# Optimization experiments

Measured on AMD Instinct MI355X. Metric: run time of the kernel, lower is better.

## Reference

```python
import jax, jax.numpy as jnp
import numpy as np

B, S, D, H, HD = 8, 1, 4096, 32, 128
MAX_SEQ, AL, FF = 2048, 10, 11008
START_POS = 2047
EPS = 1e-5


def setup_inputs() -> dict:
    key = jax.random.key(0)
    ks = jax.random.split(key, 12)
    # real RoPE angles for the single decode position START_POS
    inv_freq = 1.0 / (10000.0 ** (np.arange(0, HD, 2, dtype=np.float32) / HD))  # [HD/2]
    ang = (np.float32(START_POS) * inv_freq)[None, :]  # [S=1, HD/2]
    return {
        "x": jax.random.normal(ks[0], (B, S, D), jnp.float32),
        "adapter": jax.random.normal(ks[1], (1, AL, D), jnp.float32),
        "cache_k": jax.random.normal(ks[2], (B, MAX_SEQ, H, HD), jnp.float32),
        "cache_v": jax.random.normal(ks[3], (B, MAX_SEQ, H, HD), jnp.float32),
        "freqs_cos": jnp.cos(jnp.asarray(ang)),
        "freqs_sin": jnp.sin(jnp.asarray(ang)),
        "wq": jax.random.normal(ks[4], (D, D), jnp.float32) * 0.02,
        "wk": jax.random.normal(ks[5], (D, D), jnp.float32) * 0.02,
        "wv": jax.random.normal(ks[6], (D, D), jnp.float32) * 0.02,
        "wo": jax.random.normal(ks[7], (D, D), jnp.float32) * 0.02,
        "gate": jax.random.normal(ks[8], (1, H, 1, 1), jnp.float32) * 0.5,
        "attn_norm_w": jnp.ones((D,), jnp.float32),
        "ffn_norm_w": jnp.ones((D,), jnp.float32),
        "w1": jax.random.normal(ks[9], (D, FF), jnp.float32) * 0.02,
        "w2": jax.random.normal(ks[10], (FF, D), jnp.float32) * 0.02,
        "w3": jax.random.normal(ks[11], (D, FF), jnp.float32) * 0.02,
        "start_pos": START_POS,
    }


def _rmsnorm(x, w, eps=EPS):
    xf = x.astype(jnp.float32)
    return (xf * jax.lax.rsqrt(jnp.mean(xf * xf, axis=-1, keepdims=True) + eps)).astype(x.dtype) * w


def _rope(t, cos, sin):
    # t: [B,S,H,HD]; pairs are interleaved as in view_as_complex(reshape(..,-1,2))
    tr = t.reshape(*t.shape[:-1], HD // 2, 2)
    a, b = tr[..., 0], tr[..., 1]
    c = cos[None, :, None, :]
    s = sin[None, :, None, :]
    out = jnp.stack([a * c - b * s, a * s + b * c], axis=-1)
    return out.reshape(t.shape)


def _sdpa(q, k, v):
    # q:[B,H,S,HD], k/v:[B,H,K,HD]
    scores = jnp.einsum("bhqd,bhkd->bhqk", q, k) / jnp.sqrt(jnp.float32(HD))
    p = jax.nn.softmax(scores.astype(jnp.float32), axis=-1).astype(q.dtype)
    return jnp.einsum("bhqk,bhkd->bhqd", p, v)


def reference(x, adapter, cache_k, cache_v, freqs_cos, freqs_sin,
              wq, wk, wv, wo, gate, attn_norm_w, ffn_norm_w, w1, w2, w3, start_pos):
    bsz, seqlen, _ = x.shape
    # --- attention sub-block ---
    xn = _rmsnorm(x, attn_norm_w)
    xq = (xn @ wq).reshape(bsz, seqlen, H, HD)
    xk = (xn @ wk).reshape(bsz, seqlen, H, HD)
    xv = (xn @ wv).reshape(bsz, seqlen, H, HD)
    xq = _rope(xq, freqs_cos, freqs_sin)
    xk = _rope(xk, freqs_cos, freqs_sin)
    # KV-cache append
    cache_k = jax.lax.dynamic_update_slice(cache_k, xk, (0, start_pos, 0, 0))
    cache_v = jax.lax.dynamic_update_slice(cache_v, xv, (0, start_pos, 0, 0))
    keys = cache_k[:, : start_pos + seqlen].transpose(0, 2, 1, 3)   # [B,H,K,HD]
    values = cache_v[:, : start_pos + seqlen].transpose(0, 2, 1, 3)
    q = xq.transpose(0, 2, 1, 3)                                     # [B,H,S,HD]
    out = _sdpa(q, keys, values)                                     # [B,H,S,HD]
    # adapter-gated cross attention (adapter keys/values: no RoPE, shared over batch)
    ak = (adapter @ wk).reshape(AL, H, HD).transpose(1, 0, 2)        # [H,AL,HD]
    av = (adapter @ wv).reshape(AL, H, HD).transpose(1, 0, 2)        # [H,AL,HD]
    a_scores = jnp.einsum("bhqd,hkd->bhqk", q, ak) / jnp.sqrt(jnp.float32(HD))
    a_p = jax.nn.softmax(a_scores.astype(jnp.float32), axis=-1).astype(q.dtype)
    a_out = jnp.einsum("bhqk,hkd->bhqd", a_p, av)
    out = out + jnp.tanh(gate) * a_out
    attn_out = out.transpose(0, 2, 1, 3).reshape(bsz, seqlen, H * HD) @ wo
    h = x + attn_out
    # --- feed-forward sub-block (SwiGLU) ---
    hn = _rmsnorm(h, ffn_norm_w)
    ffn = (jax.nn.silu(hn @ w1) * (hn @ w3)) @ w2
    return h + ffn
```

## Files before the change

kernel.cpp:

```cpp
#include <hip/hip_runtime.h>
#include <cmath>

#define D_ 4096
#define H_ 32
#define HD_ 128
#define B_ 8
#define MAXSEQ_ 2048
#define AL_ 10
#define FF_ 11008
#define SCALE_ 0.08838834764831845f
#define EPS_ 1e-5f

__global__ __launch_bounds__(256) void norm_adapter_k(const float* __restrict__ x,
                                                      const float* __restrict__ w,
                                                      const float* __restrict__ adapter,
                                                      float* __restrict__ xa) {
  int b = blockIdx.x, tid = threadIdx.x;
  if (b < 8) {
    const float* xr = x + (size_t)b * D_;
    float ss = 0.f;
    for (int i = tid; i < D_; i += 256) { float v = xr[i]; ss += v * v; }
    __shared__ float red[256];
    red[tid] = ss; __syncthreads();
    for (int s = 128; s; s >>= 1) { if (tid < s) red[tid] += red[tid + s]; __syncthreads(); }
    float r = rsqrtf(red[0] / (float)D_ + EPS_);
    float* o = xa + (size_t)b * D_;
    for (int i = tid; i < D_; i += 256) o[i] = xr[i] * r * w[i];
  } else {
    int r = b - 8;
    const float4* src = (const float4*)(adapter + (size_t)r * D_);
    float4* dst = (float4*)(xa + (size_t)(8 + r) * D_);
    for (int i = tid; i < D_ / 4; i += 256) dst[i] = src[i];
  }
}

__global__ __launch_bounds__(256) void rmsnorm_k(const float* __restrict__ in,
                                                 const float* __restrict__ w,
                                                 float* __restrict__ out) {
  int b = blockIdx.x, tid = threadIdx.x;
  const float* x = in + (size_t)b * D_;
  float ss = 0.f;
  for (int i = tid; i < D_; i += 256) { float v = x[i]; ss += v * v; }
  __shared__ float red[256];
  red[tid] = ss; __syncthreads();
  for (int s = 128; s; s >>= 1) { if (tid < s) red[tid] += red[tid + s]; __syncthreads(); }
  float r = rsqrtf(red[0] / (float)D_ + EPS_);
  float* o = out + (size_t)b * D_;
  for (int i = tid; i < D_; i += 256) o[i] = x[i] * r * w[i];
}

template<int NR, int ROWS, int CHUNK, int UNROLL>
__device__ __forceinline__ void gemv_core(
    const float4* __restrict__ W4, const float (*xs)[ROWS],
    int i0, int N4, int j4, int r0, float* __restrict__ P, size_t pb, int N) {
  float4 acc[NR];
#pragma unroll
  for (int r = 0; r < NR; ++r) acc[r] = make_float4(0.f, 0.f, 0.f, 0.f);
  for (int iu = 0; iu < CHUNK; iu += UNROLL) {
    float4 w[UNROLL];
#pragma unroll
    for (int u = 0; u < UNROLL; ++u)
      w[u] = W4[(size_t)(i0 + iu + u) * N4 + j4];
#pragma unroll
    for (int u = 0; u < UNROLL; ++u) {
#pragma unroll
      for (int r = 0; r < NR; ++r) {
        float xv = xs[iu + u][r0 + r];
        acc[r].x += xv * w[u].x; acc[r].y += xv * w[u].y;
        acc[r].z += xv * w[u].z; acc[r].w += xv * w[u].w;
      }
    }
  }
#pragma unroll
  for (int r = 0; r < NR; ++r)
    *(float4*)&P[(pb + r) * (size_t)N + (size_t)4 * j4] = acc[r];
}

template<int ROWS, int RPG, int CHUNK, int UNROLL>
__global__ __launch_bounds__(256, 1) void gemv_rs(
    const float* __restrict__ X,
    const float* __restrict__ Wa, const float* __restrict__ Wb, const float* __restrict__ Wc,
    float* __restrict__ P, int N, int K) {
  const float* W = (blockIdx.z == 0) ? Wa : (blockIdx.z == 1) ? Wb : Wc;
  __shared__ float xs[CHUNK][ROWS];
  int tid = threadIdx.x;
  int i0 = blockIdx.y * CHUNK;
  for (int idx = tid; idx < ROWS * CHUNK; idx += 256) {
    int r = idx / CHUNK, ii = idx - r * CHUNK;
    xs[ii][r] = X[(size_t)r * K + i0 + ii];
  }
  __syncthreads();
  int wave = tid >> 6, lane = tid & 63;
  int r0 = wave * RPG;
  int N4 = N >> 2;
  int j4 = blockIdx.x * 64 + lane;
  const float4* W4 = (const float4*)W;
  size_t pb = ((size_t)blockIdx.z * gridDim.y + blockIdx.y) * ROWS + r0;
  constexpr int LAST = ROWS - 3 * RPG;
  if (r0 + RPG <= ROWS)
    gemv_core<RPG, ROWS, CHUNK, UNROLL>(W4, xs, i0, N4, j4, r0, P, pb, N);
  else if (LAST > 0)
    gemv_core<(LAST > 0 ? LAST : 1), ROWS, CHUNK, UNROLL>(W4, xs, i0, N4, j4, r0, P, pb, N);
}

__global__ __launch_bounds__(256) void reduce3_rope_k(
    const float* __restrict__ P, const float* __restrict__ fc, const float* __restrict__ fs,
    float* __restrict__ Ya, float* __restrict__ Yb, float* __restrict__ Yc) {
  int z = blockIdx.z;
  int i4 = blockIdx.x * 256 + threadIdx.x;
  const float4* P4 = (const float4*)P;
  size_t base = (size_t)z * 32 * 18432 + i4;
  float4 s = make_float4(0.f, 0.f, 0.f, 0.f);
#pragma unroll 8
  for (int c = 0; c < 32; ++c) {
    float4 v = P4[base + (size_t)c * 18432];
    s.x += v.x; s.y += v.y; s.z += v.z; s.w += v.w;
  }
  int row = i4 >> 10;
  if (z < 2 && row < 8) {
    int c0 = (i4 & 1023) << 2;
    int p0 = (c0 & 127) >> 1;
    float ca = fc[p0], sa = fs[p0], cb = fc[p0 + 1], sb = fs[p0 + 1];
    float4 r;
    r.x = s.x * ca - s.y * sa; r.y = s.x * sa + s.y * ca;
    r.z = s.z * cb - s.w * sb; r.w = s.z * sb + s.w * cb;
    s = r;
  }
  float4* Y = (float4*)(z == 0 ? Ya : z == 1 ? Yb : Yc);
  Y[i4] = s;
}

__global__ __launch_bounds__(256) void reduceB_k(const float* __restrict__ P,
                                                 const float* __restrict__ base,
                                                 float* __restrict__ Y, int n4, int nc) {
  int i4 = blockIdx.x * 256 + threadIdx.x;
  if (i4 >= n4) return;
  const float4* P4 = (const float4*)P;
  float4 s = ((const float4*)base)[i4];
  for (int c = 0; c < nc; ++c) {
    float4 v = P4[(size_t)c * n4 + i4];
    s.x += v.x; s.y += v.y; s.z += v.z; s.w += v.w;
  }
  ((float4*)Y)[i4] = s;
}

__global__ __launch_bounds__(256) void reduce_silu_k(const float* __restrict__ P,
                                                     float* __restrict__ gb) {
  int i4 = blockIdx.x * 256 + threadIdx.x;
  const float4* P4 = (const float4*)P;
  float4 a = make_float4(0.f, 0.f, 0.f, 0.f);
  float4 b = make_float4(0.f, 0.f, 0.f, 0.f);
#pragma unroll 8
  for (int c = 0; c < 32; ++c) {
    float4 u = P4[(size_t)c * 22016 + i4];
    float4 v = P4[(size_t)(32 + c) * 22016 + i4];
    a.x += u.x; a.y += u.y; a.z += u.z; a.w += u.w;
    b.x += v.x; b.y += v.y; b.z += v.z; b.w += v.w;
  }
  float4 o;
  o.x = (a.x / (1.f + __expf(-a.x))) * b.x;
  o.y = (a.y / (1.f + __expf(-a.y))) * b.y;
  o.z = (a.z / (1.f + __expf(-a.z))) * b.z;
  o.w = (a.w / (1.f + __expf(-a.w))) * b.w;
  ((float4*)gb)[i4] = o;
}

__global__ __launch_bounds__(256) void attn_partial(
    const float* __restrict__ qp,
    const float* __restrict__ ck,
    const float* __restrict__ cv,
    float* __restrict__ part) {
  int idx = blockIdx.x;
  int c = idx & 7, bh = idx >> 3;
  int h = bh & 31, b = bh >> 5;
  int tid = threadIdx.x, wave = tid >> 6, lane = tid & 63;
  int half = lane >> 5, l32 = lane & 31;
  bool c7 = (c == 7);
  __shared__ float sc[256];
  __shared__ float red[256];
  __shared__ float ob[4][128];
  int t0 = c * 256;
  const float4 qv = *(const float4*)&qp[(size_t)b * D_ + h * HD_ + 4 * l32];
  for (int i = 0; i < 32; ++i) {
    int tl = wave * 64 + 2 * i + half;
    int t = t0 + tl;
    const float* kptr = &ck[(((size_t)b * MAXSEQ_ + t) * H_ + h) * HD_];
    float4 kv = *(const float4*)&kptr[4 * l32];
    float s = qv.x * kv.x + qv.y * kv.y + qv.z * kv.z + qv.w * kv.w;
    s += __shfl_xor(s, 16); s += __shfl_xor(s, 8);
    s += __shfl_xor(s, 4);  s += __shfl_xor(s, 2); s += __shfl_xor(s, 1);
    if (l32 == 0) sc[tl] = (c7 && tl == 255) ? -1e30f : s * SCALE_;
  }
  __syncthreads();
  float sv = sc[tid];
  red[tid] = sv; __syncthreads();
  for (int s = 128; s; s >>= 1) { if (tid < s) red[tid] = fmaxf(red[tid], red[tid + s]); __syncthreads(); }
  float m = red[0]; __syncthreads();
  float p = __expf(sv - m);
  sc[tid] = p;
  red[tid] = p; __syncthreads();
  for (int s = 128; s; s >>= 1) { if (tid < s) red[tid] += red[tid + s]; __syncthreads(); }
  float l = red[0];
  float4 acc = make_float4(0.f, 0.f, 0.f, 0.f);
  for (int i = 0; i < 32; ++i) {
    int tl = wave * 64 + 2 * i + half;
    int t = t0 + tl;
    const float* vptr = &cv[(((size_t)b * MAXSEQ_ + t) * H_ + h) * HD_];
    float4 vv = *(const float4*)&vptr[4 * l32];
    float pp = sc[tl];
    acc.x += pp * vv.x; acc.y += pp * vv.y; acc.z += pp * vv.z; acc.w += pp * vv.w;
  }
  acc.x += __shfl_xor(acc.x, 32); acc.y += __shfl_xor(acc.y, 32);
  acc.z += __shfl_xor(acc.z, 32); acc.w += __shfl_xor(acc.w, 32);
  if (half == 0) {
    ob[wave][4 * l32 + 0] = acc.x; ob[wave][4 * l32 + 1] = acc.y;
    ob[wave][4 * l32 + 2] = acc.z; ob[wave][4 * l32 + 3] = acc.w;
  }
  __syncthreads();
  float* po = &part[(size_t)idx * 132];
  if (tid == 0) { po[0] = m; po[1] = l; }
  if (tid < 128) po[4 + tid] = ob[0][tid] + ob[1][tid] + ob[2][tid] + ob[3][tid];
}

__global__ __launch_bounds__(128) void attn_combine(
    const float* __restrict__ part,
    const float* __restrict__ qp,
    const float* __restrict__ kvk,
    const float* __restrict__ kvv,
    const float* __restrict__ gate,
    float* __restrict__ attn) {
  int bh = blockIdx.x;
  int h = bh & 31, b = bh >> 5;
  int tid = threadIdx.x;
  const float* pb = &part[(size_t)bh * 8 * 132];
  float mc[8], lc[8];
  float M = -INFINITY;
  for (int c = 0; c < 8; ++c) { mc[c] = pb[c * 132]; lc[c] = pb[c * 132 + 1]; M = fmaxf(M, mc[c]); }
  float L = 0.f, O = 0.f;
  for (int c = 0; c < 8; ++c) {
    float e = __expf(mc[c] - M);
    L += e * lc[c];
    O += e * pb[c * 132 + 4 + tid];
  }
  size_t qi = (size_t)b * D_ + h * HD_ + tid;
  float qd = qp[qi];
  __shared__ float red[128];
  __shared__ float sa[10];
  red[tid] = qd * kvk[qi]; __syncthreads();
  for (int s = 64; s; s >>= 1) { if (tid < s) red[tid] += red[tid + s]; __syncthreads(); }
  float s_new = red[0] * SCALE_;
  __syncthreads();
  float M2 = fmaxf(M, s_new);
  float eM = __expf(M - M2), eN = __expf(s_new - M2);
  L = L * eM + eN;
  O = O * eM + eN * kvv[qi];
  float main_out = O / L;
  for (int j = 0; j < 10; ++j) {
    float prod = qd * kvk[(size_t)(8 + j) * D_ + h * HD_ + tid];
    red[tid] = prod; __syncthreads();
    for (int s = 64; s; s >>= 1) { if (tid < s) red[tid] += red[tid + s]; __syncthreads(); }
    if (tid == 0) sa[j] = red[0] * SCALE_;
    __syncthreads();
  }
  float ma = -INFINITY;
  for (int j = 0; j < 10; ++j) ma = fmaxf(ma, sa[j]);
  float la = 0.f, pj[10];
  for (int j = 0; j < 10; ++j) { pj[j] = __expf(sa[j] - ma); la += pj[j]; }
  float ao = 0.f;
  for (int j = 0; j < 10; ++j) ao += pj[j] * kvv[(size_t)(8 + j) * D_ + h * HD_ + tid];
  ao /= la;
  float g = tanhf(gate[h]);
  attn[qi] = main_out + g * ao;
}

extern "C" void kernel_launch(void* const* d_in, const int* in_sizes, int n_in,
                              void* d_out, int out_size, void* d_ws, size_t ws_size,
                              hipStream_t stream) {
  (void)in_sizes; (void)n_in; (void)out_size; (void)ws_size;
  const float* x       = (const float*)d_in[0];
  const float* adapter = (const float*)d_in[1];
  const float* ck      = (const float*)d_in[2];
  const float* cv      = (const float*)d_in[3];
  const float* fc      = (const float*)d_in[4];
  const float* fs      = (const float*)d_in[5];
  const float* wq      = (const float*)d_in[6];
  const float* wk      = (const float*)d_in[7];
  const float* wv      = (const float*)d_in[8];
  const float* wo      = (const float*)d_in[9];
  const float* gate    = (const float*)d_in[10];
  const float* anw     = (const float*)d_in[11];
  const float* fnw     = (const float*)d_in[12];
  const float* w1      = (const float*)d_in[13];
  const float* w2      = (const float*)d_in[14];
  const float* w3      = (const float*)d_in[15];
  float* out = (float*)d_out;

  float* ws      = (float*)d_ws;
  float* xa      = ws;
  float* qp      = xa + 18 * D_;
  float* kp      = qp + 18 * D_;
  float* vp      = kp + 18 * D_;
  float* attn    = vp + 18 * D_;
  float* hbuf    = attn + 8 * D_;
  float* hn      = hbuf + 8 * D_;
  float* gb      = hn + 8 * D_;
  float* scratch = gb + 8 * FF_;

  norm_adapter_k<<<18, 256, 0, stream>>>(x, anw, adapter, xa);
  gemv_rs<18, 5, 128, 16><<<dim3(16, 32, 3), 256, 0, stream>>>(xa, wq, wk, wv, scratch, D_, D_);
  reduce3_rope_k<<<dim3(72, 1, 3), 256, 0, stream>>>(scratch, fc, fs, qp, kp, vp);
  attn_partial<<<2048, 256, 0, stream>>>(qp, ck, cv, scratch);
  attn_combine<<<256, 128, 0, stream>>>(scratch, qp, kp, vp, gate, attn);
  gemv_rs<8, 2, 32, 8><<<dim3(16, 128, 1), 256, 0, stream>>>(attn, wo, wo, wo, scratch, D_, D_);
  reduceB_k<<<32, 256, 0, stream>>>(scratch, x, hbuf, 8192, 128);
  rmsnorm_k<<<8, 256, 0, stream>>>(hbuf, fnw, hn);
  gemv_rs<8, 2, 128, 8><<<dim3(43, 32, 2), 256, 0, stream>>>(hn, w1, w3, w3, scratch, FF_, D_);
  reduce_silu_k<<<86, 256, 0, stream>>>(scratch, gb);
  gemv_rs<8, 2, 64, 8><<<dim3(16, 172, 1), 256, 0, stream>>>(gb, w2, w2, w2, scratch, D_, FF_);
  reduceB_k<<<32, 256, 0, stream>>>(scratch, hbuf, out, 8192, 172);
}
```

Measured before the change: 454.3 us.

## Use online softmax in attention partials and enlarge GEMV split-K chunks

The attention partial kernel is rewritten to keep a per-wave online softmax, reading K and V in a single pass with no shared-memory reductions or block barriers. Each wave writes its own partial, so the combine kernel now merges 32 partials per head. Separately, every GEMV launch gets larger K chunks and fewer split-K slices, and the reduction kernels are changed to match. This cuts partial-sum traffic and reduce work at the cost of fewer blocks for each GEMV and more partials for attention.

```diff
diff --git a/kernel.cpp b/kernel.cpp
--- a/kernel.cpp
+++ b/kernel.cpp
@@ -109,10 +109,10 @@
   int z = blockIdx.z;
   int i4 = blockIdx.x * 256 + threadIdx.x;
   const float4* P4 = (const float4*)P;
-  size_t base = (size_t)z * 32 * 18432 + i4;
+  size_t base = (size_t)z * 16 * 18432 + i4;
   float4 s = make_float4(0.f, 0.f, 0.f, 0.f);
-#pragma unroll 8
-  for (int c = 0; c < 32; ++c) {
+#pragma unroll
+  for (int c = 0; c < 16; ++c) {
     float4 v = P4[base + (size_t)c * 18432];
     s.x += v.x; s.y += v.y; s.z += v.z; s.w += v.w;
   }
@@ -150,10 +150,10 @@
   const float4* P4 = (const float4*)P;
   float4 a = make_float4(0.f, 0.f, 0.f, 0.f);
   float4 b = make_float4(0.f, 0.f, 0.f, 0.f);
-#pragma unroll 8
-  for (int c = 0; c < 32; ++c) {
+#pragma unroll
+  for (int c = 0; c < 8; ++c) {
     float4 u = P4[(size_t)c * 22016 + i4];
-    float4 v = P4[(size_t)(32 + c) * 22016 + i4];
+    float4 v = P4[(size_t)(8 + c) * 22016 + i4];
     a.x += u.x; a.y += u.y; a.z += u.z; a.w += u.w;
     b.x += v.x; b.y += v.y; b.z += v.z; b.w += v.w;
   }
@@ -175,51 +175,38 @@
   int h = bh & 31, b = bh >> 5;
   int tid = threadIdx.x, wave = tid >> 6, lane = tid & 63;
   int half = lane >> 5, l32 = lane & 31;
-  bool c7 = (c == 7);
-  __shared__ float sc[256];
-  __shared__ float red[256];
-  __shared__ float ob[4][128];
-  int t0 = c * 256;
+  int t0 = c * 256 + wave * 64;
   const float4 qv = *(const float4*)&qp[(size_t)b * D_ + h * HD_ + 4 * l32];
+  const size_t kvbase = ((size_t)b * MAXSEQ_) * (H_ * HD_) + (size_t)h * HD_ + 4 * l32;
+  float m = -INFINITY, l = 0.f;
+  float4 o = make_float4(0.f, 0.f, 0.f, 0.f);
+#pragma unroll 4
   for (int i = 0; i < 32; ++i) {
-    int tl = wave * 64 + 2 * i + half;
-    int t = t0 + tl;
-    const float* kptr = &ck[(((size_t)b * MAXSEQ_ + t) * H_ + h) * HD_];
-    float4 kv = *(const float4*)&kptr[4 * l32];
+    int t = t0 + 2 * i + half;
+    size_t off = kvbase + (size_t)t * (H_ * HD_);
+    float4 kv = *(const float4*)&ck[off];
     float s = qv.x * kv.x + qv.y * kv.y + qv.z * kv.z + qv.w * kv.w;
     s += __shfl_xor(s, 16); s += __shfl_xor(s, 8);
     s += __shfl_xor(s, 4);  s += __shfl_xor(s, 2); s += __shfl_xor(s, 1);
-    if (l32 == 0) sc[tl] = (c7 && tl == 255) ? -1e30f : s * SCALE_;
-  }
-  __syncthreads();
-  float sv = sc[tid];
-  red[tid] = sv; __syncthreads();
-  for (int s = 128; s; s >>= 1) { if (tid < s) red[tid] = fmaxf(red[tid], red[tid + s]); __syncthreads(); }
-  float m = red[0]; __syncthreads();
-  float p = __expf(sv - m);
-  sc[tid] = p;
-  red[tid] = p; __syncthreads();
-  for (int s = 128; s; s >>= 1) { if (tid < s) red[tid] += red[tid + s]; __syncthreads(); }
-  float l = red[0];
-  float4 acc = make_float4(0.f, 0.f, 0.f, 0.f);
-  for (int i = 0; i < 32; ++i) {
-    int tl = wave * 64 + 2 * i + half;
-    int t = t0 + tl;
-    const float* vptr = &cv[(((size_t)b * MAXSEQ_ + t) * H_ + h) * HD_];
-    float4 vv = *(const float4*)&vptr[4 * l32];
-    float pp = sc[tl];
-    acc.x += pp * vv.x; acc.y += pp * vv.y; acc.z += pp * vv.z; acc.w += pp * vv.w;
-  }
-  acc.x += __shfl_xor(acc.x, 32); acc.y += __shfl_xor(acc.y, 32);
-  acc.z += __shfl_xor(acc.z, 32); acc.w += __shfl_xor(acc.w, 32);
-  if (half == 0) {
-    ob[wave][4 * l32 + 0] = acc.x; ob[wave][4 * l32 + 1] = acc.y;
-    ob[wave][4 * l32 + 2] = acc.z; ob[wave][4 * l32 + 3] = acc.w;
-  }
-  __syncthreads();
-  float* po = &part[(size_t)idx * 132];
-  if (tid == 0) { po[0] = m; po[1] = l; }
-  if (tid < 128) po[4 + tid] = ob[0][tid] + ob[1][tid] + ob[2][tid] + ob[3][tid];
+    s *= SCALE_;
+    if (t == MAXSEQ_ - 1) s = -1e30f;
+    float mn = fmaxf(m, s);
+    float r = __expf(m - mn), p = __expf(s - mn);
+    float4 vv = *(const float4*)&cv[off];
+    o.x = o.x * r + p * vv.x; o.y = o.y * r + p * vv.y;
+    o.z = o.z * r + p * vv.z; o.w = o.w * r + p * vv.w;
+    l = l * r + p; m = mn;
+  }
+  float mo = __shfl_xor(m, 32);
+  float M = fmaxf(m, mo);
+  float e = __expf(m - M);
+  o.x *= e; o.y *= e; o.z *= e; o.w *= e; l *= e;
+  o.x += __shfl_xor(o.x, 32); o.y += __shfl_xor(o.y, 32);
+  o.z += __shfl_xor(o.z, 32); o.w += __shfl_xor(o.w, 32);
+  l += __shfl_xor(l, 32);
+  float* po = &part[((size_t)idx * 4 + wave) * 132];
+  if (lane == 0) { po[0] = M; po[1] = l; }
+  if (half == 0) *(float4*)&po[4 + 4 * l32] = o;
 }
 
 __global__ __launch_bounds__(128) void attn_combine(
@@ -232,14 +219,16 @@
   int bh = blockIdx.x;
   int h = bh & 31, b = bh >> 5;
   int tid = threadIdx.x;
-  const float* pb = &part[(size_t)bh * 8 * 132];
-  float mc[8], lc[8];
+  const float* pb = &part[(size_t)bh * 32 * 132];
+  __shared__ float sm[32], sl[32];
+  if (tid < 32) { sm[tid] = pb[tid * 132]; sl[tid] = pb[tid * 132 + 1]; }
+  __syncthreads();
   float M = -INFINITY;
-  for (int c = 0; c < 8; ++c) { mc[c] = pb[c * 132]; lc[c] = pb[c * 132 + 1]; M = fmaxf(M, mc[c]); }
+  for (int c = 0; c < 32; ++c) M = fmaxf(M, sm[c]);
   float L = 0.f, O = 0.f;
-  for (int c = 0; c < 8; ++c) {
-    float e = __expf(mc[c] - M);
-    L += e * lc[c];
+  for (int c = 0; c < 32; ++c) {
+    float e = __expf(sm[c] - M);
+    L += e * sl[c];
     O += e * pb[c * 132 + 4 + tid];
   }
   size_t qi = (size_t)b * D_ + h * HD_ + tid;
@@ -307,15 +296,15 @@
   float* scratch = gb + 8 * FF_;
 
   norm_adapter_k<<<18, 256, 0, stream>>>(x, anw, adapter, xa);
-  gemv_rs<18, 5, 128, 16><<<dim3(16, 32, 3), 256, 0, stream>>>(xa, wq, wk, wv, scratch, D_, D_);
+  gemv_rs<18, 5, 256, 16><<<dim3(16, 16, 3), 256, 0, stream>>>(xa, wq, wk, wv, scratch, D_, D_);
   reduce3_rope_k<<<dim3(72, 1, 3), 256, 0, stream>>>(scratch, fc, fs, qp, kp, vp);
   attn_partial<<<2048, 256, 0, stream>>>(qp, ck, cv, scratch);
   attn_combine<<<256, 128, 0, stream>>>(scratch, qp, kp, vp, gate, attn);
-  gemv_rs<8, 2, 32, 8><<<dim3(16, 128, 1), 256, 0, stream>>>(attn, wo, wo, wo, scratch, D_, D_);
-  reduceB_k<<<32, 256, 0, stream>>>(scratch, x, hbuf, 8192, 128);
+  gemv_rs<8, 2, 128, 16><<<dim3(16, 32, 1), 256, 0, stream>>>(attn, wo, wo, wo, scratch, D_, D_);
+  reduceB_k<<<32, 256, 0, stream>>>(scratch, x, hbuf, 8192, 32);
   rmsnorm_k<<<8, 256, 0, stream>>>(hbuf, fnw, hn);
-  gemv_rs<8, 2, 128, 8><<<dim3(43, 32, 2), 256, 0, stream>>>(hn, w1, w3, w3, scratch, FF_, D_);
+  gemv_rs<8, 2, 512, 16><<<dim3(43, 8, 2), 256, 0, stream>>>(hn, w1, w3, w3, scratch, FF_, D_);
   reduce_silu_k<<<86, 256, 0, stream>>>(scratch, gb);
-  gemv_rs<8, 2, 64, 8><<<dim3(16, 172, 1), 256, 0, stream>>>(gb, w2, w2, w2, scratch, D_, FF_);
-  reduceB_k<<<32, 256, 0, stream>>>(scratch, hbuf, out, 8192, 172);
-}
+  gemv_rs<8, 2, 344, 8><<<dim3(16, 32, 1), 256, 0, stream>>>(gb, w2, w2, w2, scratch, D_, FF_);
+  reduceB_k<<<32, 256, 0, stream>>>(scratch, hbuf, out, 8192, 32);
+}
```

New measurement: 398.3 us. 1.14x faster.
